# Performance work log

Measured on AMD Instinct MI355X. Metric: run time of the kernel, lower is better.

## Reference

```python
import jax, jax.numpy as jnp
import numpy as np

MIN_SCALE = 0.05
MAX_SCALE = 0.8
EPOCHS = 600
BIRTH_EPOCH = 1
NEURON_SCALE = MIN_SCALE + (MAX_SCALE - MIN_SCALE) * (BIRTH_EPOCH / EPOCHS)  # get_tide_level(1)


def setup_inputs() -> dict:
    key = jax.random.key(0)
    k1, k2, k3, k4 = jax.random.split(key, 4)
    B, T, D, N = 8, 2048, 128, 4096
    x = jax.random.normal(k1, (B, T, D), dtype=jnp.float32)
    positions = jax.random.normal(k2, (N, D), dtype=jnp.float32) * 0.5
    values = jax.random.normal(k3, (N, D), dtype=jnp.float32) * 0.02
    temperature = jax.random.uniform(k4, (N,), dtype=jnp.float32) * 0.5 + 0.25
    return {"x": x, "positions": positions, "values": values, "temperature": temperature}


def reference(x, positions, values, temperature):
    B, T, D = x.shape
    xf = x.reshape(-1, D)                                    # [M, D], M = B*T
    # Euclidean cdist via the expanded quadratic form (avoids [M,N,D] blowup)
    x2 = jnp.sum(xf * xf, axis=-1, keepdims=True)            # [M, 1]
    p2 = jnp.sum(positions * positions, axis=-1)             # [N]
    d2 = x2 + p2[None, :] - 2.0 * (xf @ positions.T)         # [M, N]
    dists = jnp.sqrt(jnp.maximum(d2, 0.0))
    effective_temp = (jnp.abs(temperature) + 0.1) * NEURON_SCALE  # [N]
    weights = jnp.exp(-dists / effective_temp[None, :])
    weights = weights / (jnp.sum(weights, axis=-1, keepdims=True) + 1e-8)
    out = weights @ values                                   # [M, D]
    return out.reshape(B, T, D)
```

## Files before the change

kernel.cpp:

```cpp
#include <hip/hip_runtime.h>
#include <hip/hip_bf16.h>


typedef __attribute__((ext_vector_type(4))) float f32x4;
typedef __attribute__((ext_vector_type(4))) int   i32x4;
typedef __attribute__((ext_vector_type(8))) int   i32x8;

#define MTOT 16384
#define NTOT 4096
#define DD   128

__device__ __forceinline__ i32x4 pack16_fp8(f32x4 a0, f32x4 a1, f32x4 a2, f32x4 a3) {
    int w0 = __builtin_amdgcn_cvt_pk_fp8_f32(a0[0], a0[1], 0, false);
    w0     = __builtin_amdgcn_cvt_pk_fp8_f32(a0[2], a0[3], w0, true);
    int w1 = __builtin_amdgcn_cvt_pk_fp8_f32(a1[0], a1[1], 0, false);
    w1     = __builtin_amdgcn_cvt_pk_fp8_f32(a1[2], a1[3], w1, true);
    int w2 = __builtin_amdgcn_cvt_pk_fp8_f32(a2[0], a2[1], 0, false);
    w2     = __builtin_amdgcn_cvt_pk_fp8_f32(a2[2], a2[3], w2, true);
    int w3 = __builtin_amdgcn_cvt_pk_fp8_f32(a3[0], a3[1], 0, false);
    w3     = __builtin_amdgcn_cvt_pk_fp8_f32(a3[2], a3[3], w3, true);
    return (i32x4){w0, w1, w2, w3};
}

__global__ __launch_bounds__(256) void tide_prep(
    const float* __restrict__ x, const float* __restrict__ pos,
    const float* __restrict__ val, const float* __restrict__ temp,
    char* __restrict__ Xb8, float* __restrict__ x2g,
    char* __restrict__ Pb8, float* __restrict__ pcg,
    float* __restrict__ outz, float* __restrict__ rsz, int* __restrict__ aflag)
{
    const int bid = blockIdx.x, tid = threadIdx.x;
    if (bid < 512) {
        const int row = bid * 32 + (tid >> 3), seg = tid & 7;
        const float* src = x + (size_t)row * DD + seg * 16;
        f32x4 a0 = ((const f32x4*)src)[0];
        f32x4 a1 = ((const f32x4*)src)[1];
        f32x4 a2 = ((const f32x4*)src)[2];
        f32x4 a3 = ((const f32x4*)src)[3];
        *(i32x4*)(Xb8 + (size_t)row * DD + seg * 16) = pack16_fp8(a0, a1, a2, a3);
        float s = a0[0]*a0[0]+a0[1]*a0[1]+a0[2]*a0[2]+a0[3]*a0[3]
                + a1[0]*a1[0]+a1[1]*a1[1]+a1[2]*a1[2]+a1[3]*a1[3]
                + a2[0]*a2[0]+a2[1]*a2[1]+a2[2]*a2[2]+a2[3]*a2[3]
                + a3[0]*a3[0]+a3[1]*a3[1]+a3[2]*a3[2]+a3[3]*a3[3];
        s += __shfl_xor(s, 1); s += __shfl_xor(s, 2); s += __shfl_xor(s, 4);
        if (seg == 0) {
            x2g[row] = s;
            if (!(s <= 400.f)) atomicOr(aflag, 1);
        }
    } else if (bid < 640) {
        const int n = (bid - 512) * 32 + (tid >> 3), seg = tid & 7;
        const float* ps = pos + (size_t)n * DD + seg * 16;
        f32x4 a0 = ((const f32x4*)ps)[0];
        f32x4 a1 = ((const f32x4*)ps)[1];
        f32x4 a2 = ((const f32x4*)ps)[2];
        f32x4 a3 = ((const f32x4*)ps)[3];
        *(i32x4*)(Pb8 + (size_t)n * DD + seg * 16) = pack16_fp8(a0, a1, a2, a3);
        float s = a0[0]*a0[0]+a0[1]*a0[1]+a0[2]*a0[2]+a0[3]*a0[3]
                + a1[0]*a1[0]+a1[1]*a1[1]+a1[2]*a1[2]+a1[3]*a1[3]
                + a2[0]*a2[0]+a2[1]*a2[1]+a2[2]*a2[2]+a2[3]*a2[3]
                + a3[0]*a3[0]+a3[1]*a3[1]+a3[2]*a3[2]+a3[3]*a3[3];
        s += __shfl_xor(s, 1); s += __shfl_xor(s, 2); s += __shfl_xor(s, 4);
        if (seg == 0) {
            if (!(s <= 100.f)) atomicOr(aflag, 1);
            float efft = (fabsf(temp[n]) + 0.1f) * 0.05125f;
            float thr = 106.7459f * efft;
            float pcv = s - thr * thr - 32.0f;
            pcg[n] = pcv;
            if (!isfinite(pcv)) atomicOr(aflag, 1);
        }
        const float* vs = val + (size_t)n * DD + seg * 16;
        f32x4 b0 = ((const f32x4*)vs)[0];
        f32x4 b1 = ((const f32x4*)vs)[1];
        f32x4 b2 = ((const f32x4*)vs)[2];
        f32x4 b3 = ((const f32x4*)vs)[3];
        float vchk = fabsf(b0[0])+fabsf(b0[1])+fabsf(b0[2])+fabsf(b0[3])
                   + fabsf(b1[0])+fabsf(b1[1])+fabsf(b1[2])+fabsf(b1[3])
                   + fabsf(b2[0])+fabsf(b2[1])+fabsf(b2[2])+fabsf(b2[3])
                   + fabsf(b3[0])+fabsf(b3[1])+fabsf(b3[2])+fabsf(b3[3]);
        if (!isfinite(vchk)) atomicOr(aflag, 1);
    } else if (bid < 1152) {
        f32x4 z = {0.f, 0.f, 0.f, 0.f};
        float* dst = outz + (size_t)(bid - 640) * 4096;
        #pragma unroll
        for (int j = 0; j < 4; ++j)
            *(f32x4*)(dst + (size_t)(tid + 256 * j) * 4) = z;
    } else {
        f32x4 z = {0.f, 0.f, 0.f, 0.f};
        float* dst = rsz + (size_t)(bid - 1152) * 4096;
        #pragma unroll
        for (int j = 0; j < 4; ++j)
            *(f32x4*)(dst + (size_t)(tid + 256 * j) * 4) = z;
        if (bid == 1152 && tid == 0) aflag[0] = 0;
    }
}

__global__ __launch_bounds__(256, 4) void tide_main(
    const char* __restrict__ Xb8, const float* __restrict__ x2g,
    const char* __restrict__ Pb8, const float* __restrict__ pcg,
    const float* __restrict__ x, const float* __restrict__ pos,
    const float* __restrict__ val, const float* __restrict__ temp,
    float* __restrict__ rsum_g, float* __restrict__ oaccum,
    const int* __restrict__ aflagp)
{
    __shared__ __attribute__((aligned(16))) char xpanel[128 * DD];
    __shared__ __attribute__((aligned(16))) float x2t[128];

    const int tid = threadIdx.x;
    const int wid = tid >> 6, lane = tid & 63;
    const int lo = lane & 15, hi = lane >> 4;
    const int nb = blockIdx.x & 15, mc = blockIdx.x >> 4;
    const int mb = mc * 128;
    const int c0 = nb * 256 + wid * 64;
    const int sc = 0x7F7F7F7F;

    i32x8 pf8[4];
    float pc[4];
    #pragma unroll
    for (int f = 0; f < 4; ++f) {
        const char* pb = Pb8 + (size_t)(c0 + f * 16 + lo) * DD + hi * 32;
        i32x4 plo = *(const i32x4*)pb;
        i32x4 phi = *(const i32x4*)(pb + 16);
        pf8[f] = (i32x8){plo[0], plo[1], plo[2], plo[3],
                         phi[0], phi[1], phi[2], phi[3]};
        pc[f] = pcg[c0 + f * 16 + lo];
    }
    const int af = aflagp[0];

    const int srow = tid >> 3, sch = tid & 7;
    const char* xs = Xb8 + (size_t)(mb + srow) * DD + ((sch ^ (srow & 7)) * 16);
    char* ld = xpanel + tid * 16;
    #pragma unroll
    for (int i = 0; i < 4; ++i)
        __builtin_amdgcn_global_load_lds(
            (const __attribute__((address_space(1))) void*)(xs + (size_t)i * 32 * DD),
            (__attribute__((address_space(3))) void*)(ld + i * 4096), 16, 0, 0);
    if (tid < 128) x2t[tid] = x2g[mb + tid];
    __syncthreads();

    float em[4] = {3.4e38f, 3.4e38f, 3.4e38f, 3.4e38f};

    #pragma unroll
    for (int t = 0; t < 8; ++t) {
        const char* xb = xpanel + (t * 16 + lo) * DD;
        i32x4 xa = *(const i32x4*)(xb + (((hi * 2)     ^ (lo & 7)) * 16));
        i32x4 xc = *(const i32x4*)(xb + (((hi * 2 + 1) ^ (lo & 7)) * 16));
        i32x8 xf8 = (i32x8){xa[0], xa[1], xa[2], xa[3],
                            xc[0], xc[1], xc[2], xc[3]};
        f32x4 x2r = *(const f32x4*)(x2t + t * 16 + hi * 4);

        f32x4 s0 = __builtin_amdgcn_mfma_scale_f32_16x16x128_f8f6f4(
            xf8, pf8[0], (f32x4){0.f,0.f,0.f,0.f}, 0, 0, 0, sc, 0, sc);
        f32x4 s1 = __builtin_amdgcn_mfma_scale_f32_16x16x128_f8f6f4(
            xf8, pf8[1], (f32x4){0.f,0.f,0.f,0.f}, 0, 0, 0, sc, 0, sc);
        f32x4 s2 = __builtin_amdgcn_mfma_scale_f32_16x16x128_f8f6f4(
            xf8, pf8[2], (f32x4){0.f,0.f,0.f,0.f}, 0, 0, 0, sc, 0, sc);
        f32x4 s3 = __builtin_amdgcn_mfma_scale_f32_16x16x128_f8f6f4(
            xf8, pf8[3], (f32x4){0.f,0.f,0.f,0.f}, 0, 0, 0, sc, 0, sc);

        #pragma unroll
        for (int r = 0; r < 4; ++r) {
            float e0 = fmaf(s0[r], -2.f, x2r[r] + pc[0]);
            float e1 = fmaf(s1[r], -2.f, x2r[r] + pc[1]);
            float e2 = fmaf(s2[r], -2.f, x2r[r] + pc[2]);
            float e3 = fmaf(s3[r], -2.f, x2r[r] + pc[3]);
            em[0] = fminf(em[0], e0); em[1] = fminf(em[1], e1);
            em[2] = fminf(em[2], e2); em[3] = fminf(em[3], e3);
        }
    }

    const float emin = fminf(fminf(em[0], em[1]), fminf(em[2], em[3]));
    const int bad = (!(emin >= 0.f)) | af;
    if (__builtin_expect(__any(bad), 0)) {
        #pragma unroll 1
        for (int t = 0; t < 8; ++t) {
            #pragma unroll 1
            for (int f = 0; f < 4; ++f) {
                const int n = c0 + f * 16 + lo;
                float efft = (fabsf(temp[n]) + 0.1f) * 0.05125f;
                #pragma unroll 1
                for (int r = 0; r < 4; ++r) {
                    const int m = mb + t * 16 + hi * 4 + r;
                    float dot = 0.f, p2 = 0.f;
                    const float* xr = x + (size_t)m * DD;
                    const float* pr = pos + (size_t)n * DD;
                    #pragma unroll 4
                    for (int k = 0; k < DD; k += 4) {
                        f32x4 xv = *(const f32x4*)(xr + k);
                        f32x4 pv = *(const f32x4*)(pr + k);
                        dot = fmaf(xv[0], pv[0], dot); dot = fmaf(xv[1], pv[1], dot);
                        dot = fmaf(xv[2], pv[2], dot); dot = fmaf(xv[3], pv[3], dot);
                        p2  = fmaf(pv[0], pv[0], p2);  p2  = fmaf(pv[1], pv[1], p2);
                        p2  = fmaf(pv[2], pv[2], p2);  p2  = fmaf(pv[3], pv[3], p2);
                    }
                    float d2 = fmaxf(x2t[m - mb] + p2 - 2.f * dot, 0.f);
                    float wv = expf(-__builtin_amdgcn_sqrtf(d2) / efft);
                    if (wv != 0.f || af) {
                        atomicAdd(&rsum_g[m], wv);
                        const float* vr = val + (size_t)n * DD;
                        #pragma unroll 1
                        for (int dcol = 0; dcol < DD; ++dcol)
                            atomicAdd(&oaccum[(size_t)m * DD + dcol], wv * vr[dcol]);
                    }
                }
            }
        }
    }
}

__global__ __launch_bounds__(256) void tide_norm(
    const float* __restrict__ rsum_g, float* __restrict__ outp)
{
    const int row = blockIdx.x * 256 + threadIdx.x;
    float s = rsum_g[row];
    if (s != 0.f) {
        float inv = 1.f / (s + 1e-8f);
        float* p = outp + (size_t)row * DD;
        #pragma unroll 4
        for (int j = 0; j < DD / 4; ++j) {
            f32x4 v = *(f32x4*)(p + j * 4);
            v[0] *= inv; v[1] *= inv; v[2] *= inv; v[3] *= inv;
            *(f32x4*)(p + j * 4) = v;
        }
    }
}

extern "C" void kernel_launch(void* const* d_in, const int* in_sizes, int n_in,
                              void* d_out, int out_size, void* d_ws, size_t ws_size,
                              hipStream_t stream) {
    const float* x    = (const float*)d_in[0];
    const float* pos  = (const float*)d_in[1];
    const float* val  = (const float*)d_in[2];
    const float* temp = (const float*)d_in[3];
    float* out = (float*)d_out;

    char* ws = (char*)d_ws;
    char*  Xb8    = ws;
    char*  Pb8    = ws + 2097152;
    float* x2g    = (float*)(ws + 2621440);
    float* pcg    = (float*)(ws + 2686976);
    float* rsum_g = (float*)(ws + 2703360);
    int*   aflag  = (int*)  (ws + 2768896);

    hipLaunchKernelGGL(tide_prep, dim3(1156), dim3(256), 0, stream,
                       x, pos, val, temp, Xb8, x2g, Pb8, pcg, out, rsum_g, aflag);
    hipLaunchKernelGGL(tide_main, dim3(2048), dim3(256), 0, stream,
                       Xb8, x2g, Pb8, pcg, x, pos, val, temp, rsum_g, out, aflag);
    hipLaunchKernelGGL(tide_norm, dim3(64), dim3(256), 0, stream,
                       rsum_g, out);
}
```

Baseline: 23.64 us.

## Fuse x fp8 quantization and norm computation into main kernel

Moves the conversion of x to fp8 and the row-norm computation out of the prep kernel and into tide_main. Each block now loads its own fp32 x rows, packs them into the swizzled LDS panel and computes x2 and the anomaly flag locally, so the fp8 X workspace is no longer written and read back. The cost is that each x panel is now read and converted 16 times, once per N-block, instead of once in prep. The main kernel also loses its async global-to-LDS load and gains an extra barrier.

```diff
diff --git a/kernel.cpp b/kernel.cpp
--- a/kernel.cpp
+++ b/kernel.cpp
@@ -23,32 +23,14 @@
 }
 
 __global__ __launch_bounds__(256) void tide_prep(
-    const float* __restrict__ x, const float* __restrict__ pos,
-    const float* __restrict__ val, const float* __restrict__ temp,
-    char* __restrict__ Xb8, float* __restrict__ x2g,
+    const float* __restrict__ pos, const float* __restrict__ val,
+    const float* __restrict__ temp,
     char* __restrict__ Pb8, float* __restrict__ pcg,
     float* __restrict__ outz, float* __restrict__ rsz, int* __restrict__ aflag)
 {
     const int bid = blockIdx.x, tid = threadIdx.x;
-    if (bid < 512) {
-        const int row = bid * 32 + (tid >> 3), seg = tid & 7;
-        const float* src = x + (size_t)row * DD + seg * 16;
-        f32x4 a0 = ((const f32x4*)src)[0];
-        f32x4 a1 = ((const f32x4*)src)[1];
-        f32x4 a2 = ((const f32x4*)src)[2];
-        f32x4 a3 = ((const f32x4*)src)[3];
-        *(i32x4*)(Xb8 + (size_t)row * DD + seg * 16) = pack16_fp8(a0, a1, a2, a3);
-        float s = a0[0]*a0[0]+a0[1]*a0[1]+a0[2]*a0[2]+a0[3]*a0[3]
-                + a1[0]*a1[0]+a1[1]*a1[1]+a1[2]*a1[2]+a1[3]*a1[3]
-                + a2[0]*a2[0]+a2[1]*a2[1]+a2[2]*a2[2]+a2[3]*a2[3]
-                + a3[0]*a3[0]+a3[1]*a3[1]+a3[2]*a3[2]+a3[3]*a3[3];
-        s += __shfl_xor(s, 1); s += __shfl_xor(s, 2); s += __shfl_xor(s, 4);
-        if (seg == 0) {
-            x2g[row] = s;
-            if (!(s <= 400.f)) atomicOr(aflag, 1);
-        }
-    } else if (bid < 640) {
-        const int n = (bid - 512) * 32 + (tid >> 3), seg = tid & 7;
+    if (bid < 128) {
+        const int n = bid * 32 + (tid >> 3), seg = tid & 7;
         const float* ps = pos + (size_t)n * DD + seg * 16;
         f32x4 a0 = ((const f32x4*)ps)[0];
         f32x4 a1 = ((const f32x4*)ps)[1];
@@ -78,32 +60,33 @@
                    + fabsf(b2[0])+fabsf(b2[1])+fabsf(b2[2])+fabsf(b2[3])
                    + fabsf(b3[0])+fabsf(b3[1])+fabsf(b3[2])+fabsf(b3[3]);
         if (!isfinite(vchk)) atomicOr(aflag, 1);
-    } else if (bid < 1152) {
+    } else if (bid < 384) {
         f32x4 z = {0.f, 0.f, 0.f, 0.f};
-        float* dst = outz + (size_t)(bid - 640) * 4096;
+        float* dst = outz + (size_t)(bid - 128) * 8192;
+        #pragma unroll
+        for (int j = 0; j < 8; ++j)
+            *(f32x4*)(dst + (size_t)j * 1024 + tid * 4) = z;
+    } else {
+        f32x4 z = {0.f, 0.f, 0.f, 0.f};
+        float* dst = rsz + (size_t)(bid - 384) * 4096;
         #pragma unroll
         for (int j = 0; j < 4; ++j)
-            *(f32x4*)(dst + (size_t)(tid + 256 * j) * 4) = z;
-    } else {
-        f32x4 z = {0.f, 0.f, 0.f, 0.f};
-        float* dst = rsz + (size_t)(bid - 1152) * 4096;
-        #pragma unroll
-        for (int j = 0; j < 4; ++j)
-            *(f32x4*)(dst + (size_t)(tid + 256 * j) * 4) = z;
-        if (bid == 1152 && tid == 0) aflag[0] = 0;
+            *(f32x4*)(dst + (size_t)j * 1024 + tid * 4) = z;
+        if (bid == 384 && tid == 0) aflag[0] = 0;
     }
 }
 
 __global__ __launch_bounds__(256, 4) void tide_main(
-    const char* __restrict__ Xb8, const float* __restrict__ x2g,
+    const float* __restrict__ x,
     const char* __restrict__ Pb8, const float* __restrict__ pcg,
-    const float* __restrict__ x, const float* __restrict__ pos,
-    const float* __restrict__ val, const float* __restrict__ temp,
+    const float* __restrict__ pos, const float* __restrict__ val,
+    const float* __restrict__ temp,
     float* __restrict__ rsum_g, float* __restrict__ oaccum,
     const int* __restrict__ aflagp)
 {
     __shared__ __attribute__((aligned(16))) char xpanel[128 * DD];
     __shared__ __attribute__((aligned(16))) float x2t[128];
+    __shared__ int lds_bad;
 
     const int tid = threadIdx.x;
     const int wid = tid >> 6, lane = tid & 63;
@@ -112,6 +95,8 @@
     const int mb = mc * 128;
     const int c0 = nb * 256 + wid * 64;
     const int sc = 0x7F7F7F7F;
+
+    if (tid == 0) lds_bad = 0;
 
     i32x8 pf8[4];
     float pc[4];
@@ -124,18 +109,33 @@
                          phi[0], phi[1], phi[2], phi[3]};
         pc[f] = pcg[c0 + f * 16 + lo];
     }
-    const int af = aflagp[0];
+
+    __syncthreads();
 
     const int srow = tid >> 3, sch = tid & 7;
-    const char* xs = Xb8 + (size_t)(mb + srow) * DD + ((sch ^ (srow & 7)) * 16);
+    const int csrc = sch ^ (srow & 7);
     char* ld = xpanel + tid * 16;
     #pragma unroll
-    for (int i = 0; i < 4; ++i)
-        __builtin_amdgcn_global_load_lds(
-            (const __attribute__((address_space(1))) void*)(xs + (size_t)i * 32 * DD),
-            (__attribute__((address_space(3))) void*)(ld + i * 4096), 16, 0, 0);
-    if (tid < 128) x2t[tid] = x2g[mb + tid];
+    for (int i = 0; i < 4; ++i) {
+        const int row = srow + 32 * i;
+        const float* src = x + (size_t)(mb + row) * DD + csrc * 16;
+        f32x4 a0 = ((const f32x4*)src)[0];
+        f32x4 a1 = ((const f32x4*)src)[1];
+        f32x4 a2 = ((const f32x4*)src)[2];
+        f32x4 a3 = ((const f32x4*)src)[3];
+        *(i32x4*)(ld + i * 4096) = pack16_fp8(a0, a1, a2, a3);
+        float s = a0[0]*a0[0]+a0[1]*a0[1]+a0[2]*a0[2]+a0[3]*a0[3]
+                + a1[0]*a1[0]+a1[1]*a1[1]+a1[2]*a1[2]+a1[3]*a1[3]
+                + a2[0]*a2[0]+a2[1]*a2[1]+a2[2]*a2[2]+a2[3]*a2[3]
+                + a3[0]*a3[0]+a3[1]*a3[1]+a3[2]*a3[2]+a3[3]*a3[3];
+        s += __shfl_xor(s, 1); s += __shfl_xor(s, 2); s += __shfl_xor(s, 4);
+        if (sch == 0) {
+            x2t[row] = s;
+            if (!(s <= 400.f)) lds_bad = 1;
+        }
+    }
     __syncthreads();
+    const int af = aflagp[0] | lds_bad;
 
     float em[4] = {3.4e38f, 3.4e38f, 3.4e38f, 3.4e38f};
 
@@ -234,17 +234,15 @@
     float* out = (float*)d_out;
 
     char* ws = (char*)d_ws;
-    char*  Xb8    = ws;
-    char*  Pb8    = ws + 2097152;
-    float* x2g    = (float*)(ws + 2621440);
-    float* pcg    = (float*)(ws + 2686976);
-    float* rsum_g = (float*)(ws + 2703360);
-    int*   aflag  = (int*)  (ws + 2768896);
-
-    hipLaunchKernelGGL(tide_prep, dim3(1156), dim3(256), 0, stream,
-                       x, pos, val, temp, Xb8, x2g, Pb8, pcg, out, rsum_g, aflag);
+    char*  Pb8    = ws;
+    float* pcg    = (float*)(ws + 524288);
+    float* rsum_g = (float*)(ws + 540672);
+    int*   aflag  = (int*)  (ws + 606208);
+
+    hipLaunchKernelGGL(tide_prep, dim3(388), dim3(256), 0, stream,
+                       pos, val, temp, Pb8, pcg, out, rsum_g, aflag);
     hipLaunchKernelGGL(tide_main, dim3(2048), dim3(256), 0, stream,
-                       Xb8, x2g, Pb8, pcg, x, pos, val, temp, rsum_g, out, aflag);
+                       x, Pb8, pcg, pos, val, temp, rsum_g, out, aflag);
     hipLaunchKernelGGL(tide_norm, dim3(64), dim3(256), 0, stream,
                        rsum_g, out);
 }
```

Result: slower. 30.32 us (+28.3%).
